# Performance work log

Hardware: AMD Instinct MI355X
Metric: run time of the kernel (lower is better)

The kernel has to match this reference:

```python
import jax, jax.numpy as jnp
import numpy as np

# ---- equation / net constants (mirrors eqn_config / net_config) ----
NT = 256
DT = 0.04
N_HIST = 64
HIDDEN = 512
LAMBD = 1.0
MU1 = 0.08
MU2 = 0.02
R = 0.02
SIGMA = 0.2
BETA = 0.1
ETA = 0.5
LOGEPS = 1e-6
UTIL_PENALTY = 100.0
GEOMETRIC_SUM = (1.0 - np.exp(-LAMBD * DT * (N_HIST - 1))) / LAMBD  # discounted weight on oldest point
FINAL_DISC = float(np.exp(-BETA * NT * DT))


def setup_inputs() -> dict:
    key = jax.random.key(0)
    k = jax.random.split(key, 9)
    B = 16384
    dw_sample = jax.random.normal(k[0], (B, NT), dtype=jnp.float32) * np.sqrt(DT)
    x_init = jax.random.uniform(k[1], (B, N_HIST), dtype=jnp.float32) + 0.5  # positive initial wealth path
    # exponential kernel over the delay window (most recent point has weight ~1)
    exp_array = jnp.exp(-LAMBD * DT * jnp.arange(N_HIST - 1, 0, -1, dtype=jnp.float32))
    s1 = 1.0 / np.sqrt(N_HIST)
    s2 = 1.0 / np.sqrt(HIDDEN)
    W1 = jax.random.normal(k[2], (N_HIST, HIDDEN), dtype=jnp.float32) * s1
    b1 = jnp.zeros((HIDDEN,), dtype=jnp.float32)
    W2 = jax.random.normal(k[3], (HIDDEN, HIDDEN), dtype=jnp.float32) * s2
    b2 = jnp.zeros((HIDDEN,), dtype=jnp.float32)
    W3 = jax.random.normal(k[4], (HIDDEN, 2), dtype=jnp.float32) * s2
    b3 = jnp.zeros((2,), dtype=jnp.float32)
    return {"dw_sample": dw_sample, "x_init": x_init, "exp_array": exp_array,
            "W1": W1, "b1": b1, "W2": W2, "b2": b2, "W3": W3, "b3": b3}


def reference(dw_sample, x_init, exp_array, W1, b1, W2, b2, W3, b3):
    def util(v):  # log-utility with floor (util_tf)
        return jnp.log(jax.nn.relu(v) + LOGEPS)

    def policy(x_hist):  # feedforward policy on the history window; final_pi_tf = 2*sigmoid
        h = jax.nn.relu(x_hist @ W1 + b1)
        h = jax.nn.relu(h @ W2 + b2)
        return 2.0 * jax.nn.sigmoid(h @ W3 + b3)  # [B, 2]

    x = x_init[:, -1]                       # [B]
    x_hist0 = x_init                        # [B, N_HIST]
    y0 = jnp.sum(exp_array * x_init[:, 1:], axis=-1) * DT + GEOMETRIC_SUM * x_init[:, 0]
    reward0 = jnp.zeros_like(x)

    discounts = jnp.exp(-BETA * DT * jnp.arange(NT, dtype=jnp.float32))  # exp(-beta*t*dt)

    def step(carry, inputs):
        x, y, x_hist, reward = carry
        dw_t, disc = inputs                 # dw_t: [B], disc: scalar
        pi = policy(x_hist)                 # [B, 2]
        inst_r = util(pi[:, 0] * x) * disc - jax.nn.relu(-x) * UTIL_PENALTY
        reward = reward + inst_r * DT
        dx = ((MU1 - R) * pi[:, 1] - pi[:, 0] + R) * x + MU2 * y
        x_new = x + dx * DT + SIGMA * x * pi[:, 1] * dw_t
        y_new = y * jnp.exp(-DT * LAMBD) + x_new * DT
        x_hist_new = jnp.concatenate([x_hist[:, 1:], x_new[:, None]], axis=-1)
        return (x_new, y_new, x_hist_new, reward), None

    (x, y, _, reward), _ = jax.lax.scan(
        step, (x, y0, x_hist0, reward0), (dw_sample.T, discounts))

    # terminal step t == nt
    reward = reward + util(x + ETA * y) / BETA * FINAL_DISC
    reward = reward - jax.nn.relu(-x) * UTIL_PENALTY
    return -reward
```

## Files before the change

kernel.cpp:

```cpp
#include <hip/hip_runtime.h>
#include <stdint.h>
#include <stddef.h>

#define NTS 256

typedef short bf16x8 __attribute__((ext_vector_type(8)));
typedef short bf16x4 __attribute__((ext_vector_type(4)));
typedef float f32x4 __attribute__((ext_vector_type(4)));
typedef float f32x2 __attribute__((ext_vector_type(2)));

__device__ __forceinline__ unsigned short f2bf(float f) {
  union { float f; unsigned u; } c; c.f = f;
  unsigned u = c.u;
  u += 0x7fffu + ((u >> 16) & 1u);
  return (unsigned short)(u >> 16);
}

__global__ __launch_bounds__(256) void prep_weights(const float* __restrict__ W1,
                                                    const float* __restrict__ W2,
                                                    unsigned short* __restrict__ wp) {
  int gid = blockIdx.x * 256 + threadIdx.x;
  if (gid >= 294912) return;
  int e = gid & 7, lane = (gid >> 3) & 63, fb = (gid >> 9) & 31, pan = gid >> 14;
  int q = lane >> 4, j = lane & 15, f = fb * 16 + j;
  float v;
  if (pan < 2) v = W1[(pan * 32 + q * 8 + e) * 512 + f];
  else         v = W2[((pan - 2) * 32 + q * 8 + e) * 512 + f];
  wp[gid] = f2bf(v);
}

__device__ __forceinline__ void stage_panel(const unsigned short* __restrict__ wp,
                                            int pan, char* dst_base, int wv, int lane) {
#pragma unroll
  for (int i = 0; i < 4; ++i) {
    const unsigned short* g = wp + (size_t)pan * 16384 + (wv * 4 + i) * 512 + lane * 8;
    char* l = dst_base + wv * 4096 + i * 1024;
    __builtin_amdgcn_global_load_lds((const __attribute__((address_space(1))) void*)g,
                                     (__attribute__((address_space(3))) void*)l,
                                     16, 0, 0);
  }
}

__global__ __launch_bounds__(512, 2) void po_fused(
    const float* __restrict__ dw, const float* __restrict__ x_init,
    const float* __restrict__ exp_arr, const float* __restrict__ b1,
    const float* __restrict__ b2, const float* __restrict__ W3,
    const float* __restrict__ b3, const unsigned short* __restrict__ wp,
    float* __restrict__ out) {
  extern __shared__ char smem[];
  char* const w1L = smem;
  char* const h1C = smem + 65536;
  char* const histC = smem + 131072;
  unsigned int* const h0L = (unsigned int*)(smem + 139264);
  float* const piL = (float*)(smem + 141312);
  float* const dwL = (float*)(smem + 145408);
  unsigned short* const xnbL = (unsigned short*)(smem + 149504);
  float* const b1L = (float*)(smem + 149632);
  float* const b2L = (float*)(smem + 151680);
  float* const w3L = (float*)(smem + 153728);

  const int tid = threadIdx.x;
  const int lane = tid & 63;
  const int wv = tid >> 6;
  const int q = lane >> 4;
  const int j = lane & 15;
  const int wg = blockIdx.x;

  b1L[tid] = b1[tid];
  b2L[tid] = b2[tid];
  w3L[tid] = W3[tid];
  w3L[tid + 512] = W3[tid + 512];

  {
    int ntp = tid >> 6;
    int p0 = ntp >> 2, nt0 = ntp & 3;
    int b = nt0 * 16 + j, k0 = p0 * 32 + q * 8;
    const float* src = x_init + ((size_t)wg * 64 + b) * 64 + k0;
    bf16x8 v;
#pragma unroll
    for (int e = 0; e < 8; ++e) v[e] = (short)f2bf(src[e]);
    *(bf16x8*)(histC + tid * 16) = v;
    h0L[tid] = (unsigned int)(unsigned short)v[0];
  }

  float xreg = 0.f, yreg = 0.f, rreg = 0.f;
  if (tid < 64) {
    const float* row = x_init + ((size_t)wg * 64 + tid) * 64;
    float y0 = 0.f;
    for (int k = 0; k < 63; ++k) y0 += exp_arr[k] * row[1 + k];
    y0 = y0 * 0.04f + (1.f - __expf(-2.52f)) * row[0];
    xreg = row[63];
    yreg = y0;
  }
  const float b30 = b3[0], b31 = b3[1];

  stage_panel(wp, 0, w1L, wv, lane);
  stage_panel(wp, 1, w1L + 32768, wv, lane);

  const unsigned short* const wpW2 = wp + 2 * 16384;
  const int wfo = wv * 2048 + lane * 8;

  bf16x8 wA[4], wB[4];
#pragma unroll
  for (int mt = 0; mt < 4; ++mt)
    wA[mt] = *(const bf16x8*)(wpW2 + wfo + mt * 512);

  __syncthreads();

  f32x4 acc[4][4];

#pragma unroll 1
  for (int t = 0; t < NTS; ++t) {
    if ((t & 15) == 0) {
      int b = tid >> 3, c = tid & 7;
      f32x2 v = *(const f32x2*)(dw + ((size_t)wg * 64 + b) * NTS + t + c * 2);
      dwL[(c * 2) * 64 + b] = v[0];
      dwL[(c * 2 + 1) * 64 + b] = v[1];
    }

#pragma unroll
    for (int mt = 0; mt < 4; ++mt)
#pragma unroll
      for (int nt = 0; nt < 4; ++nt) acc[mt][nt] = (f32x4){0.f, 0.f, 0.f, 0.f};
#pragma unroll
    for (int p = 0; p < 2; ++p) {
      const char* pb = w1L + p * 32768 + wv * 4096;
#pragma unroll
      for (int nt = 0; nt < 4; ++nt) {
        bf16x8 bfr = *(const bf16x8*)(histC + ((p * 4 + nt) * 64 + lane) * 16);
#pragma unroll
        for (int mt = 0; mt < 4; ++mt) {
          bf16x8 afr = *(const bf16x8*)(pb + mt * 1024 + lane * 16);
          acc[mt][nt] = __builtin_amdgcn_mfma_f32_16x16x32_bf16(afr, bfr,
                                                                acc[mt][nt], 0, 0, 0);
        }
      }
    }
#pragma unroll
    for (int mt = 0; mt < 4; ++mt) {
      int f0 = wv * 64 + mt * 16 + q * 4;
      int wb = ((f0 >> 5) * 256 + ((f0 >> 3) & 3) * 16 + j) * 16 + (f0 & 7) * 2;
#pragma unroll
      for (int nt = 0; nt < 4; ++nt) {
        bf16x4 pk;
#pragma unroll
        for (int r = 0; r < 4; ++r)
          pk[r] = (short)f2bf(fmaxf(acc[mt][nt][r] + b1L[f0 + r], 0.f));
        *(bf16x4*)(h1C + wb + nt * 1024) = pk;
      }
    }
    __syncthreads();

#pragma unroll
    for (int mt = 0; mt < 4; ++mt)
#pragma unroll
      for (int nt = 0; nt < 4; ++nt) acc[mt][nt] = (f32x4){0.f, 0.f, 0.f, 0.f};
    {
      const unsigned short* pb = wpW2;
      const char* h1p = h1C;
#pragma unroll 1
      for (int kk = 0; kk < 8; ++kk) {
#pragma unroll
        for (int mt = 0; mt < 4; ++mt)
          wB[mt] = *(const bf16x8*)(pb + 16384 + wfo + mt * 512);
#pragma unroll
        for (int nt = 0; nt < 4; ++nt) {
          bf16x8 bfr = *(const bf16x8*)(h1p + nt * 1024 + lane * 16);
#pragma unroll
          for (int mt = 0; mt < 4; ++mt)
            acc[mt][nt] = __builtin_amdgcn_mfma_f32_16x16x32_bf16(wA[mt], bfr,
                                                                  acc[mt][nt], 0, 0, 0);
        }
        {
          const unsigned short* pn = (kk == 7) ? wpW2 : (pb + 32768);
#pragma unroll
          for (int mt = 0; mt < 4; ++mt)
            wA[mt] = *(const bf16x8*)(pn + wfo + mt * 512);
        }
#pragma unroll
        for (int nt = 0; nt < 4; ++nt) {
          bf16x8 bfr = *(const bf16x8*)(h1p + 4096 + nt * 1024 + lane * 16);
#pragma unroll
          for (int mt = 0; mt < 4; ++mt)
            acc[mt][nt] = __builtin_amdgcn_mfma_f32_16x16x32_bf16(wB[mt], bfr,
                                                                  acc[mt][nt], 0, 0, 0);
        }
        pb += 32768;
        h1p += 8192;
      }
    }

#pragma unroll
    for (int nt = 0; nt < 4; ++nt) {
      float p0a = 0.f, p1a = 0.f;
#pragma unroll
      for (int mt = 0; mt < 4; ++mt) {
        int f0 = wv * 64 + mt * 16 + q * 4;
#pragma unroll
        for (int r = 0; r < 4; ++r) {
          float v = fmaxf(acc[mt][nt][r] + b2L[f0 + r], 0.f);
          p0a += v * w3L[(f0 + r) * 2];
          p1a += v * w3L[(f0 + r) * 2 + 1];
        }
      }
      p0a += __shfl_xor(p0a, 16); p0a += __shfl_xor(p0a, 32);
      p1a += __shfl_xor(p1a, 16); p1a += __shfl_xor(p1a, 32);
      if (q == 0) {
        int b = nt * 16 + j;
        piL[(wv * 64 + b) * 2] = p0a;
        piL[(wv * 64 + b) * 2 + 1] = p1a;
      }
    }
    __syncthreads();

    bf16x8 hown = *(const bf16x8*)(histC + tid * 16);
    int pIdx = (tid >> 8) & 1;
    bool fromX = (q == 3) && (pIdx == 1);
    unsigned short hlast = 0;
    if (!fromX) {
      int idx2 = (q < 3) ? tid + 16 : tid + 208;
      hlast = (unsigned short)h0L[idx2];
    }

    if (tid < 64) {
      float z0 = b30, z1 = b31;
#pragma unroll
      for (int w = 0; w < 8; ++w) {
        z0 += piL[(w * 64 + tid) * 2];
        z1 += piL[(w * 64 + tid) * 2 + 1];
      }
      float pi0 = 2.f / (1.f + __expf(-z0));
      float pi1 = 2.f / (1.f + __expf(-z1));
      float x = xreg, y = yreg;
      float disc = __expf(-0.004f * (float)t);
      float rv = fmaxf(pi0 * x, 0.f) + 1e-6f;
      rreg += (__logf(rv) * disc - fmaxf(-x, 0.f) * 100.f) * 0.04f;
      float dwv = dwL[(t & 15) * 64 + tid];
      float dxv = (0.06f * pi1 - pi0 + 0.02f) * x + 0.02f * y;
      float xn = x + dxv * 0.04f + 0.2f * x * pi1 * dwv;
      yreg = y * 0.960789439152323f + xn * 0.04f;
      xreg = xn;
      xnbL[tid] = f2bf(xn);
    }
    __syncthreads();

    {
      int b = ((tid >> 6) & 3) * 16 + j;
      bf16x8 nw;
#pragma unroll
      for (int e = 0; e < 7; ++e) nw[e] = hown[e + 1];
      nw[7] = fromX ? (short)xnbL[b] : (short)hlast;
      *(bf16x8*)(histC + tid * 16) = nw;
      h0L[tid] = (unsigned int)(unsigned short)nw[0];
    }
    __syncthreads();
  }

  if (tid < 64) {
    float rw = rreg + __logf(fmaxf(xreg + 0.5f * yreg, 0.f) + 1e-6f) * 10.f * __expf(-1.024f);
    rw -= fmaxf(-xreg, 0.f) * 100.f;
    out[(size_t)wg * 64 + tid] = -rw;
  }
}

extern "C" void kernel_launch(void* const* d_in, const int* in_sizes, int n_in,
                              void* d_out, int out_size, void* d_ws, size_t ws_size,
                              hipStream_t stream) {
  const float* dw      = (const float*)d_in[0];
  const float* x_init  = (const float*)d_in[1];
  const float* exp_arr = (const float*)d_in[2];
  const float* W1      = (const float*)d_in[3];
  const float* b1      = (const float*)d_in[4];
  const float* W2      = (const float*)d_in[5];
  const float* b2      = (const float*)d_in[6];
  const float* W3      = (const float*)d_in[7];
  const float* b3      = (const float*)d_in[8];
  unsigned short* wp = (unsigned short*)d_ws;
  float* out = (float*)d_out;

  (void)hipFuncSetAttribute((const void*)po_fused,
                            hipFuncAttributeMaxDynamicSharedMemorySize, 160 * 1024);

  prep_weights<<<1152, 256, 0, stream>>>(W1, W2, wp);
  po_fused<<<256, 512, 157824, stream>>>(dw, x_init, exp_arr, b1, b2, W3, b3, wp, out);
}
```

Baseline: 2.376 ms.

## Remove per-step barrier by redundant recurrence per wave and double-buffered history

Every wave now computes the scalar recurrence for all 64 batch rows redundantly, so the xn value reaches each wave through a shuffle instead of LDS. A double-buffered h0 array plus wave shuffles for the neighbour history element let one __syncthreads per timestep be dropped. It also reorders layer-1 MFMA loops to reuse B fragments, vectorises the bias and W3 loads, splits pi partials into two arrays, and raises wave priority around the layer-2 MFMA blocks. The cost is redundant transcendental work in all 8 waves and slightly more LDS.

After: 2.271 ms. 1.05x faster.

```diff
diff --git a/kernel.cpp b/kernel.cpp
--- a/kernel.cpp
+++ b/kernel.cpp
@@ -52,12 +52,12 @@
   char* const h1C = smem + 65536;
   char* const histC = smem + 131072;
   unsigned int* const h0L = (unsigned int*)(smem + 139264);
-  float* const piL = (float*)(smem + 141312);
-  float* const dwL = (float*)(smem + 145408);
-  unsigned short* const xnbL = (unsigned short*)(smem + 149504);
-  float* const b1L = (float*)(smem + 149632);
-  float* const b2L = (float*)(smem + 151680);
-  float* const w3L = (float*)(smem + 153728);
+  float* const p0L = (float*)(smem + 143360);
+  float* const p1L = (float*)(smem + 145408);
+  float* const dwL = (float*)(smem + 147456);
+  float* const b1L = (float*)(smem + 151552);
+  float* const b2L = (float*)(smem + 153600);
+  float* const w3L = (float*)(smem + 155648);
 
   const int tid = threadIdx.x;
   const int lane = tid & 63;
@@ -71,11 +71,10 @@
   w3L[tid] = W3[tid];
   w3L[tid + 512] = W3[tid + 512];
 
+  const int b_h = (wv & 3) * 16 + j;
   {
-    int ntp = tid >> 6;
-    int p0 = ntp >> 2, nt0 = ntp & 3;
-    int b = nt0 * 16 + j, k0 = p0 * 32 + q * 8;
-    const float* src = x_init + ((size_t)wg * 64 + b) * 64 + k0;
+    const int k0 = (wv >> 2) * 32 + q * 8;
+    const float* src = x_init + ((size_t)wg * 64 + b_h) * 64 + k0;
     bf16x8 v;
 #pragma unroll
     for (int e = 0; e < 8; ++e) v[e] = (short)f2bf(src[e]);
@@ -83,21 +82,20 @@
     h0L[tid] = (unsigned int)(unsigned short)v[0];
   }
 
-  float xreg = 0.f, yreg = 0.f, rreg = 0.f;
-  if (tid < 64) {
-    const float* row = x_init + ((size_t)wg * 64 + tid) * 64;
+  float xreg, yreg, rreg = 0.f;
+  {
+    const float* row = x_init + ((size_t)wg * 64 + lane) * 64;
     float y0 = 0.f;
     for (int k = 0; k < 63; ++k) y0 += exp_arr[k] * row[1 + k];
-    y0 = y0 * 0.04f + (1.f - __expf(-2.52f)) * row[0];
+    yreg = y0 * 0.04f + (1.f - __expf(-2.52f)) * row[0];
     xreg = row[63];
-    yreg = y0;
   }
   const float b30 = b3[0], b31 = b3[1];
 
   stage_panel(wp, 0, w1L, wv, lane);
   stage_panel(wp, 1, w1L + 32768, wv, lane);
 
-  const unsigned short* const wpW2 = wp + 2 * 16384;
+  const unsigned short* const wpW2 = wp + 32768;
   const int wfo = wv * 2048 + lane * 8;
 
   bf16x8 wA[4], wB[4];
@@ -125,27 +123,30 @@
 #pragma unroll
     for (int p = 0; p < 2; ++p) {
       const char* pb = w1L + p * 32768 + wv * 4096;
-#pragma unroll
-      for (int nt = 0; nt < 4; ++nt) {
-        bf16x8 bfr = *(const bf16x8*)(histC + ((p * 4 + nt) * 64 + lane) * 16);
-#pragma unroll
-        for (int mt = 0; mt < 4; ++mt) {
-          bf16x8 afr = *(const bf16x8*)(pb + mt * 1024 + lane * 16);
-          acc[mt][nt] = __builtin_amdgcn_mfma_f32_16x16x32_bf16(afr, bfr,
+      bf16x8 bfr[4];
+#pragma unroll
+      for (int nt = 0; nt < 4; ++nt)
+        bfr[nt] = *(const bf16x8*)(histC + ((p * 4 + nt) * 64 + lane) * 16);
+#pragma unroll
+      for (int mt = 0; mt < 4; ++mt) {
+        bf16x8 afr = *(const bf16x8*)(pb + mt * 1024 + lane * 16);
+#pragma unroll
+        for (int nt = 0; nt < 4; ++nt)
+          acc[mt][nt] = __builtin_amdgcn_mfma_f32_16x16x32_bf16(afr, bfr[nt],
                                                                 acc[mt][nt], 0, 0, 0);
-        }
       }
     }
 #pragma unroll
     for (int mt = 0; mt < 4; ++mt) {
       int f0 = wv * 64 + mt * 16 + q * 4;
+      f32x4 b1v = *(const f32x4*)(b1L + f0);
       int wb = ((f0 >> 5) * 256 + ((f0 >> 3) & 3) * 16 + j) * 16 + (f0 & 7) * 2;
 #pragma unroll
       for (int nt = 0; nt < 4; ++nt) {
         bf16x4 pk;
 #pragma unroll
         for (int r = 0; r < 4; ++r)
-          pk[r] = (short)f2bf(fmaxf(acc[mt][nt][r] + b1L[f0 + r], 0.f));
+          pk[r] = (short)f2bf(fmaxf(acc[mt][nt][r] + b1v[r], 0.f));
         *(bf16x4*)(h1C + wb + nt * 1024) = pk;
       }
     }
@@ -163,6 +164,7 @@
 #pragma unroll
         for (int mt = 0; mt < 4; ++mt)
           wB[mt] = *(const bf16x8*)(pb + 16384 + wfo + mt * 512);
+        __builtin_amdgcn_s_setprio(1);
 #pragma unroll
         for (int nt = 0; nt < 4; ++nt) {
           bf16x8 bfr = *(const bf16x8*)(h1p + nt * 1024 + lane * 16);
@@ -171,12 +173,14 @@
             acc[mt][nt] = __builtin_amdgcn_mfma_f32_16x16x32_bf16(wA[mt], bfr,
                                                                   acc[mt][nt], 0, 0, 0);
         }
+        __builtin_amdgcn_s_setprio(0);
         {
           const unsigned short* pn = (kk == 7) ? wpW2 : (pb + 32768);
 #pragma unroll
           for (int mt = 0; mt < 4; ++mt)
             wA[mt] = *(const bf16x8*)(pn + wfo + mt * 512);
         }
+        __builtin_amdgcn_s_setprio(1);
 #pragma unroll
         for (int nt = 0; nt < 4; ++nt) {
           bf16x8 bfr = *(const bf16x8*)(h1p + 4096 + nt * 1024 + lane * 16);
@@ -185,49 +189,53 @@
             acc[mt][nt] = __builtin_amdgcn_mfma_f32_16x16x32_bf16(wB[mt], bfr,
                                                                   acc[mt][nt], 0, 0, 0);
         }
+        __builtin_amdgcn_s_setprio(0);
         pb += 32768;
         h1p += 8192;
       }
     }
 
-#pragma unroll
-    for (int nt = 0; nt < 4; ++nt) {
-      float p0a = 0.f, p1a = 0.f;
+    {
+      float p0a[4] = {0.f, 0.f, 0.f, 0.f};
+      float p1a[4] = {0.f, 0.f, 0.f, 0.f};
 #pragma unroll
       for (int mt = 0; mt < 4; ++mt) {
         int f0 = wv * 64 + mt * 16 + q * 4;
-#pragma unroll
-        for (int r = 0; r < 4; ++r) {
-          float v = fmaxf(acc[mt][nt][r] + b2L[f0 + r], 0.f);
-          p0a += v * w3L[(f0 + r) * 2];
-          p1a += v * w3L[(f0 + r) * 2 + 1];
-        }
-      }
-      p0a += __shfl_xor(p0a, 16); p0a += __shfl_xor(p0a, 32);
-      p1a += __shfl_xor(p1a, 16); p1a += __shfl_xor(p1a, 32);
-      if (q == 0) {
-        int b = nt * 16 + j;
-        piL[(wv * 64 + b) * 2] = p0a;
-        piL[(wv * 64 + b) * 2 + 1] = p1a;
+        f32x4 b2v = *(const f32x4*)(b2L + f0);
+        f32x4 w3a = *(const f32x4*)(w3L + f0 * 2);
+        f32x4 w3b = *(const f32x4*)(w3L + f0 * 2 + 4);
+#pragma unroll
+        for (int nt = 0; nt < 4; ++nt) {
+          float v0 = fmaxf(acc[mt][nt][0] + b2v[0], 0.f);
+          float v1 = fmaxf(acc[mt][nt][1] + b2v[1], 0.f);
+          float v2 = fmaxf(acc[mt][nt][2] + b2v[2], 0.f);
+          float v3 = fmaxf(acc[mt][nt][3] + b2v[3], 0.f);
+          p0a[nt] += v0 * w3a[0] + v1 * w3a[2] + v2 * w3b[0] + v3 * w3b[2];
+          p1a[nt] += v0 * w3a[1] + v1 * w3a[3] + v2 * w3b[1] + v3 * w3b[3];
+        }
+      }
+#pragma unroll
+      for (int nt = 0; nt < 4; ++nt) {
+        p0a[nt] += __shfl_xor(p0a[nt], 16);
+        p0a[nt] += __shfl_xor(p0a[nt], 32);
+        p1a[nt] += __shfl_xor(p1a[nt], 16);
+        p1a[nt] += __shfl_xor(p1a[nt], 32);
+        if (q == 0) {
+          int b = nt * 16 + j;
+          p0L[wv * 64 + b] = p0a[nt];
+          p1L[wv * 64 + b] = p1a[nt];
+        }
       }
     }
     __syncthreads();
 
-    bf16x8 hown = *(const bf16x8*)(histC + tid * 16);
-    int pIdx = (tid >> 8) & 1;
-    bool fromX = (q == 3) && (pIdx == 1);
-    unsigned short hlast = 0;
-    if (!fromX) {
-      int idx2 = (q < 3) ? tid + 16 : tid + 208;
-      hlast = (unsigned short)h0L[idx2];
-    }
-
-    if (tid < 64) {
+    float xn;
+    {
       float z0 = b30, z1 = b31;
 #pragma unroll
       for (int w = 0; w < 8; ++w) {
-        z0 += piL[(w * 64 + tid) * 2];
-        z1 += piL[(w * 64 + tid) * 2 + 1];
+        z0 += p0L[w * 64 + lane];
+        z1 += p1L[w * 64 + lane];
       }
       float pi0 = 2.f / (1.f + __expf(-z0));
       float pi1 = 2.f / (1.f + __expf(-z1));
@@ -235,23 +243,32 @@
       float disc = __expf(-0.004f * (float)t);
       float rv = fmaxf(pi0 * x, 0.f) + 1e-6f;
       rreg += (__logf(rv) * disc - fmaxf(-x, 0.f) * 100.f) * 0.04f;
-      float dwv = dwL[(t & 15) * 64 + tid];
+      float dwv = dwL[(t & 15) * 64 + lane];
       float dxv = (0.06f * pi1 - pi0 + 0.02f) * x + 0.02f * y;
-      float xn = x + dxv * 0.04f + 0.2f * x * pi1 * dwv;
+      xn = x + dxv * 0.04f + 0.2f * x * pi1 * dwv;
       yreg = y * 0.960789439152323f + xn * 0.04f;
       xreg = xn;
-      xnbL[tid] = f2bf(xn);
-    }
-    __syncthreads();
+    }
 
     {
-      int b = ((tid >> 6) & 3) * 16 + j;
+      bf16x8 own = *(const bf16x8*)(histC + tid * 16);
+      int e0 = (int)(unsigned short)own[0];
+      int nbr = __shfl_down(e0, 16);
+      float xb = __shfl(xn, b_h);
+      unsigned short xbf = f2bf(xb);
+      unsigned short last;
+      if (q == 3) {
+        last = (wv >= 4) ? xbf
+                         : (unsigned short)h0L[(t & 1) * 512 + tid + 208];
+      } else {
+        last = (unsigned short)nbr;
+      }
       bf16x8 nw;
 #pragma unroll
-      for (int e = 0; e < 7; ++e) nw[e] = hown[e + 1];
-      nw[7] = fromX ? (short)xnbL[b] : (short)hlast;
+      for (int e = 0; e < 7; ++e) nw[e] = own[e + 1];
+      nw[7] = (short)last;
       *(bf16x8*)(histC + tid * 16) = nw;
-      h0L[tid] = (unsigned int)(unsigned short)nw[0];
+      h0L[((t + 1) & 1) * 512 + tid] = (unsigned int)(unsigned short)nw[0];
     }
     __syncthreads();
   }
@@ -282,5 +299,5 @@
                             hipFuncAttributeMaxDynamicSharedMemorySize, 160 * 1024);
 
   prep_weights<<<1152, 256, 0, stream>>>(W1, W2, wp);
-  po_fused<<<256, 512, 157824, stream>>>(dw, x_init, exp_arr, b1, b2, W3, b3, wp, out);
-}
+  po_fused<<<256, 512, 159744, stream>>>(dw, x_init, exp_arr, b1, b2, W3, b3, wp, out);
+}
```
